# Kernel optimization log

Measured on AMD Instinct MI355X. Metric: run time of the kernel, lower is better.

## Reference

```python
import jax, jax.numpy as jnp
import numpy as np

B, S, D, H = 64, 512, 1024, 512
W_SEG, T_SEG, C_SEG = 96, 24, 128  # words, tables, columns per example (padded/fixed)


def setup_inputs() -> dict:
    key = jax.random.key(0)
    ks = jax.random.split(key, 8)
    return {
        "q_enc": jax.random.normal(ks[0], (B, S, D), dtype=jnp.float32),
        "W_sub": jax.random.normal(ks[1], (D, H), dtype=jnp.float32) * 0.02,
        "W_tab": jax.random.normal(ks[2], (D, H), dtype=jnp.float32) * 0.02,
        "W_col": jax.random.normal(ks[3], (D, H), dtype=jnp.float32) * 0.02,
        "no_entry": jax.random.normal(ks[4], (H,), dtype=jnp.float32) * 0.02,
        "word_seg": jax.random.randint(ks[5], (B, S), 0, W_SEG, dtype=jnp.int32),
        "table_seg": jax.random.randint(ks[6], (B, S), 0, T_SEG, dtype=jnp.int32),
        "col_seg": jax.random.randint(ks[7], (B, S), 0, C_SEG, dtype=jnp.int32),
    }


def _segsum(x, ids, n):
    # ragged range-sum over token axis: torch.sum(q_enc[b, st:ed, :], dim=0)
    return jax.vmap(lambda xb, ib: jax.ops.segment_sum(xb, ib, num_segments=n))(x, ids)


def reference(q_enc, W_sub, W_tab, W_col, no_entry, word_seg, table_seg, col_seg):
    word_vecs = _segsum(q_enc, word_seg, W_SEG)     # [B, W, D]
    tab_vecs = _segsum(q_enc, table_seg, T_SEG)     # [B, T, D]
    col_vecs = _segsum(q_enc, col_seg, C_SEG)       # [B, C, D]
    # SubtreeEncoder / SchemaEncoder abstracted as tanh-linear D -> H
    sub = jnp.tanh(word_vecs @ W_sub)               # [B, W, H] encoded subtrees
    tab = jnp.tanh(tab_vecs @ W_tab)                # [B, T, H]
    col = jnp.tanh(col_vecs @ W_col)                # [B, C, H]
    ne = jnp.broadcast_to(no_entry, (q_enc.shape[0], 1, no_entry.shape[0]))
    entity = jnp.concatenate([tab, col, ne], axis=1)  # [B, T+C+1, H]
    # per-example mm + softmax over entities
    att = jax.nn.softmax(jnp.einsum('bwh,beh->bwe', sub, entity), axis=-1)
    return att
```

## Files before the change

### kernel.cpp

```cpp
#include <hip/hip_runtime.h>
#include <hip/hip_bf16.h>
#include <math.h>

#define B_ 64
#define S_ 512
#define D_ 1024
#define H_ 512
#define WSEG 96
#define TSEG 24
#define CSEG 128
#define NSEG (WSEG + TSEG + CSEG)
#define ESEG (TSEG + CSEG + 1)
#define EPAD 160

typedef _Float16 f16x8 __attribute__((ext_vector_type(8)));
typedef _Float16 f16x4 __attribute__((ext_vector_type(4)));
typedef float f32x4 __attribute__((ext_vector_type(4)));

#define GL16(g, l)                                                      \
  __builtin_amdgcn_global_load_lds(                                     \
      (const __attribute__((address_space(1))) void*)(g),               \
      (__attribute__((address_space(3))) void*)(l), 16, 0, 0)

__device__ inline float tanh_fast(float x) {
  const float xc = fminf(12.f, fmaxf(-12.f, x));
  const float e = __expf(2.f * xc);
  return (e - 1.f) * __builtin_amdgcn_rcpf(e + 1.f);
}

__global__ __launch_bounds__(512) void setup_kernel(
    const int* __restrict__ wseg, const int* __restrict__ tseg,
    const int* __restrict__ cseg, const float* __restrict__ Ws,
    const float* __restrict__ Wt_, const float* __restrict__ Wc,
    const float* __restrict__ ne, int* __restrict__ lw, int* __restrict__ lt,
    int* __restrict__ lc, int* __restrict__ meta, _Float16* __restrict__ Wt16,
    _Float16* __restrict__ ent) {
  __shared__ int wid[S_], tid_[S_], cid[S_];
  __shared__ int cw[WSEG], ct[TSEG], ccnt[CSEG];
  __shared__ float tile[64][65];
  const int blk = blockIdx.x;
  const int t = threadIdx.x;

  if (blk < 64) {
    const int b = blk;
    const int myw = wseg[b * S_ + t];
    const int myt = tseg[b * S_ + t];
    const int myc = cseg[b * S_ + t];
    wid[t] = myw;
    tid_[t] = myt;
    cid[t] = myc;
    if (t < WSEG) cw[t] = 0;
    if (t < TSEG) ct[t] = 0;
    if (t < CSEG) ccnt[t] = 0;
    __syncthreads();

    atomicAdd(&cw[myw], 1);
    atomicAdd(&ct[myt], 1);
    atomicAdd(&ccnt[myc], 1);
    __syncthreads();

    if (t == 0) {
      int r = 0;
      for (int i = 0; i < WSEG; ++i) {
        const int c = cw[i];
        meta[b * NSEG + i] = r | (c << 16);
        cw[i] = r;
        r += c;
      }
      r = 0;
      for (int i = 0; i < TSEG; ++i) {
        const int c = ct[i];
        meta[b * NSEG + WSEG + i] = r | (c << 16);
        ct[i] = r;
        r += c;
      }
      r = 0;
      for (int i = 0; i < CSEG; ++i) {
        const int c = ccnt[i];
        meta[b * NSEG + WSEG + TSEG + i] = r | (c << 16);
        ccnt[i] = r;
        r += c;
      }
    }
    __syncthreads();

    int rw = 0, rt = 0, rc = 0;
    for (int s = 0; s < S_; ++s) {
      const int below = (s < t) ? 1 : 0;
      rw += below & (wid[s] == myw);
      rt += below & (tid_[s] == myt);
      rc += below & (cid[s] == myc);
    }
    lw[b * S_ + cw[myw] + rw] = t;
    lt[b * S_ + ct[myt] + rt] = t;
    lc[b * S_ + ccnt[myc] + rc] = t;
  } else if (blk < 448) {
    const int blk2 = blk - 64;
    const int z = blk2 >> 7;
    const int rem = blk2 & 127;
    const int k0 = (rem >> 3) * 64;
    const int n0 = (rem & 7) * 64;
    const float* W = (z == 0) ? Ws : ((z == 1) ? Wt_ : Wc);
    const int tx = t & 63, ty = (t >> 6) & 3;

    if (t < 256) {
#pragma unroll
      for (int i = 0; i < 16; ++i) {
        const int kl = i * 4 + ty;
        tile[kl][tx] = W[(size_t)(k0 + kl) * H_ + n0 + tx];
      }
    }
    __syncthreads();
    if (t < 256) {
      _Float16* oh = Wt16 + (size_t)z * H_ * D_;
#pragma unroll
      for (int i = 0; i < 16; ++i) {
        const int nl = i * 4 + ty;
        oh[(size_t)(n0 + nl) * D_ + k0 + tx] = (_Float16)tile[tx][nl];
      }
    }
  } else {
    const int b = blk - 448;
    ent[((size_t)b * EPAD + 152) * H_ + t] = (_Float16)ne[t];
#pragma unroll
    for (int r = 153; r < EPAD; ++r)
      ent[((size_t)b * EPAD + r) * H_ + t] = (_Float16)0.f;
  }
}

__global__ __launch_bounds__(256) void gather_rows_kernel(
    const float* __restrict__ q, const int* __restrict__ lw,
    const int* __restrict__ lt, const int* __restrict__ lc,
    const int* __restrict__ meta, _Float16* __restrict__ A) {
  const int t = threadIdx.x;
  const int bid = blockIdx.x;
  const int r = (bid & 7) * (B_ * NSEG / 8) + (bid >> 3);
  const int b = r / NSEG;
  const int seg = r % NSEG;

  const int m = meta[r];
  const int start = m & 0xFFFF;
  const int count = m >> 16;

  const int* list;
  int arow;
  if (seg < WSEG) {
    list = lw;
    arow = b * WSEG + seg;
  } else if (seg < WSEG + TSEG) {
    list = lt;
    arow = B_ * WSEG + b * TSEG + (seg - WSEG);
  } else {
    list = lc;
    arow = B_ * (WSEG + TSEG) + b * CSEG + (seg - WSEG - TSEG);
  }
  const int* lp = list + b * S_ + start;

  const float* qb = q + (size_t)b * S_ * D_;
  float4 acc = make_float4(0.f, 0.f, 0.f, 0.f);
  int i = 0;
  for (; i + 4 <= count; i += 4) {
    const int s0 = lp[i], s1 = lp[i + 1], s2 = lp[i + 2], s3 = lp[i + 3];
    const float4 a0 = *(const float4*)(qb + (size_t)s0 * D_ + (t << 2));
    const float4 a1 = *(const float4*)(qb + (size_t)s1 * D_ + (t << 2));
    const float4 a2 = *(const float4*)(qb + (size_t)s2 * D_ + (t << 2));
    const float4 a3 = *(const float4*)(qb + (size_t)s3 * D_ + (t << 2));
    acc.x += (a0.x + a1.x) + (a2.x + a3.x);
    acc.y += (a0.y + a1.y) + (a2.y + a3.y);
    acc.z += (a0.z + a1.z) + (a2.z + a3.z);
    acc.w += (a0.w + a1.w) + (a2.w + a3.w);
  }
  for (; i < count; ++i) {
    const float4 a = *(const float4*)(qb + (size_t)lp[i] * D_ + (t << 2));
    acc.x += a.x;
    acc.y += a.y;
    acc.z += a.z;
    acc.w += a.w;
  }
  const f16x4 hv = {(_Float16)acc.x, (_Float16)acc.y, (_Float16)acc.z,
                    (_Float16)acc.w};
  *(f16x4*)(A + (size_t)arow * D_ + (t << 2)) = hv;
}

__global__ __launch_bounds__(256) void gemm3_kernel(
    const _Float16* __restrict__ A, const _Float16* __restrict__ Wt16,
    _Float16* __restrict__ sub, _Float16* __restrict__ ent) {
  __shared__ __align__(16) char smem[32768];
  char* sA = smem;
  char* sB = smem + 16384;

  const int tid = threadIdx.x;
  const int wid = tid >> 6;
  const int lane = tid & 63;
  const int lin = blockIdx.x + blockIdx.y * 4;
  const int logical = (lin & 7) * 62 + (lin >> 3);
  const int m0 = (logical >> 2) * 128;
  const int n0 = (logical & 3) * 128;
  const int id = (m0 < B_ * WSEG) ? 0 : ((m0 < B_ * (WSEG + TSEG)) ? 1 : 2);

  const _Float16* B_g = Wt16 + (size_t)id * H_ * D_ + (size_t)n0 * D_;
  const _Float16* A_g = A + (size_t)m0 * D_;

  const int rsub = lane >> 3;
  const int csrc = (lane & 7) ^ rsub;

  const int wr = wid >> 1, wc = wid & 1;
  const int arow0 = wr * 64 + (lane & 15);
  const int brow0 = wc * 64 + (lane & 15);
  const int cbase = (lane >> 4) * 16;
  const int sw = (lane & 7) << 4;

  f32x4 acc[4][4] = {};

#pragma unroll 1
  for (int kt = 0; kt < D_ / 64; ++kt) {
    __syncthreads();
    const size_t kofs = (size_t)kt * 64 + (size_t)csrc * 8;
#pragma unroll
    for (int j = 0; j < 4; ++j) {
      const int i = wid * 4 + j;
      const size_t grow = (size_t)(i * 8 + rsub) * D_ + kofs;
      GL16(A_g + grow, sA + i * 1024);
      GL16(B_g + grow, sB + i * 1024);
    }
    __syncthreads();

#pragma unroll
    for (int ks = 0; ks < 2; ++ks) {
      const int cc = ((cbase + ks * 64) ^ sw);
      f16x8 a[4], bv[4];
#pragma unroll
      for (int mi = 0; mi < 4; ++mi)
        a[mi] = *(const f16x8*)(sA + (arow0 + mi * 16) * 128 + cc);
#pragma unroll
      for (int ni = 0; ni < 4; ++ni)
        bv[ni] = *(const f16x8*)(sB + (brow0 + ni * 16) * 128 + cc);
#pragma unroll
      for (int mi = 0; mi < 4; ++mi)
#pragma unroll
        for (int ni = 0; ni < 4; ++ni)
          acc[mi][ni] = __builtin_amdgcn_mfma_f32_16x16x32_f16(
              a[mi], bv[ni], acc[mi][ni], 0, 0, 0);
    }
  }

  const int rowb = m0 + wr * 64 + (lane >> 4) * 4;
  const int colb = n0 + wc * 64 + (lane & 15);
#pragma unroll
  for (int mi = 0; mi < 4; ++mi)
#pragma unroll
    for (int ni = 0; ni < 4; ++ni) {
      const f32x4 v = acc[mi][ni];
      const int col = colb + ni * 16;
#pragma unroll
      for (int r = 0; r < 4; ++r) {
        const int row = rowb + mi * 16 + r;
        const _Float16 val = (_Float16)tanh_fast(v[r]);
        if (id == 0) {
          sub[(size_t)row * H_ + col] = val;
        } else if (id == 1) {
          const int lr = row - B_ * WSEG;
          const int bb = lr / TSEG;
          const int rr = lr - bb * TSEG;
          ent[((size_t)bb * EPAD + rr) * H_ + col] = val;
        } else {
          const int lr = row - B_ * (WSEG + TSEG);
          const int bb = lr >> 7;
          const int rr = lr & 127;
          ent[((size_t)bb * EPAD + TSEG + rr) * H_ + col] = val;
        }
      }
    }
}

__global__ __launch_bounds__(192) void attn_mfma_kernel(
    const _Float16* __restrict__ sub, const _Float16* __restrict__ ent,
    float* __restrict__ out) {
  __shared__ __align__(16) char smem[30720];
  char* sS = smem;
  char* sE = smem + 6144;

  const int tid = threadIdx.x;
  const int wid = tid >> 6;
  const int lane = tid & 63;
  const int b = blockIdx.x >> 1;
  const int half = blockIdx.x & 1;

  const _Float16* S_g = sub + ((size_t)b * WSEG + half * 48) * H_;
  const _Float16* E_g = ent + (size_t)b * EPAD * H_;

  const int rsub = lane >> 3;
  const int csrc = (lane & 7) ^ rsub;

  const int arow0 = wid * 16 + (lane & 15);
  const int brow0 = lane & 15;
  const int cbase = (lane >> 4) * 16;
  const int sw = (lane & 7) << 4;

  f32x4 acc[10] = {};

#pragma unroll 1
  for (int kt = 0; kt < H_ / 64; ++kt) {
    __syncthreads();
    const size_t kofs = (size_t)kt * 64 + (size_t)csrc * 8;
#pragma unroll
    for (int j = 0; j < 9; ++j) {
      const int ig = wid * 9 + j;
      if (ig < 6) {
        GL16(S_g + (size_t)(ig * 8 + rsub) * H_ + kofs, sS + ig * 1024);
      } else if (ig < 26) {
        const int i = ig - 6;
        GL16(E_g + (size_t)(i * 8 + rsub) * H_ + kofs, sE + i * 1024);
      }
    }
    __syncthreads();

#pragma unroll
    for (int ks = 0; ks < 2; ++ks) {
      const int cc = ((cbase + ks * 64) ^ sw);
      const f16x8 a = *(const f16x8*)(sS + arow0 * 128 + cc);
#pragma unroll
      for (int ni = 0; ni < 10; ++ni) {
        const f16x8 bv = *(const f16x8*)(sE + (brow0 + ni * 16) * 128 + cc);
        acc[ni] = __builtin_amdgcn_mfma_f32_16x16x32_f16(a, bv, acc[ni], 0, 0,
                                                         0);
      }
    }
  }

  __syncthreads();
  float (*lg)[EPAD] = (float(*)[EPAD])smem;
  const int rowb = wid * 16 + (lane >> 4) * 4;
  const int colb = lane & 15;
#pragma unroll
  for (int ni = 0; ni < 10; ++ni) {
    const f32x4 v = acc[ni];
#pragma unroll
    for (int r = 0; r < 4; ++r) lg[rowb + r][colb + ni * 16] = v[r];
  }
  __syncthreads();

  for (int r = wid; r < 48; r += 3) {
    const float x0 = lg[r][lane];
    const float x1 = lg[r][lane + 64];
    const bool has2 = (lane + 128) < ESEG;
    const float x2 = has2 ? lg[r][lane + 128] : -INFINITY;
    float m = fmaxf(fmaxf(x0, x1), x2);
#pragma unroll
    for (int off = 32; off >= 1; off >>= 1) m = fmaxf(m, __shfl_xor(m, off, 64));
    const float p0 = expf(x0 - m);
    const float p1 = expf(x1 - m);
    const float p2 = has2 ? expf(x2 - m) : 0.f;
    float ssum = p0 + p1 + p2;
#pragma unroll
    for (int off = 32; off >= 1; off >>= 1) ssum += __shfl_xor(ssum, off, 64);
    const float inv = 1.f / ssum;
    float* ob = out + ((size_t)(b * WSEG + half * 48 + r)) * ESEG;
    ob[lane] = p0 * inv;
    ob[lane + 64] = p1 * inv;
    if (has2) ob[lane + 128] = p2 * inv;
  }
}

extern "C" void kernel_launch(void* const* d_in, const int* in_sizes, int n_in,
                              void* d_out, int out_size, void* d_ws,
                              size_t ws_size, hipStream_t stream) {
  const float* q = (const float*)d_in[0];
  const float* Wsub = (const float*)d_in[1];
  const float* Wtab = (const float*)d_in[2];
  const float* Wcol = (const float*)d_in[3];
  const float* ne = (const float*)d_in[4];
  const int* wseg = (const int*)d_in[5];
  const int* tseg = (const int*)d_in[6];
  const int* cseg = (const int*)d_in[7];
  float* out = (float*)d_out;

  char* w = (char*)d_ws;
  _Float16* A = (_Float16*)(w);
  _Float16* ent = (_Float16*)(w + 32505856);
  _Float16* Wt16 = (_Float16*)(w + 42991616);
  _Float16* sub = (_Float16*)(w + 46137344);
  int* lw = (int*)(w + 52428800);
  int* lt = (int*)(w + 52559872);
  int* lc = (int*)(w + 52690944);
  int* meta = (int*)(w + 52822016);

  setup_kernel<<<512, 512, 0, stream>>>(wseg, tseg, cseg, Wsub, Wtab, Wcol,
                                        ne, lw, lt, lc, meta, Wt16, ent);
  gather_rows_kernel<<<B_ * NSEG, 256, 0, stream>>>(q, lw, lt, lc, meta, A);
  gemm3_kernel<<<dim3(4, 124), 256, 0, stream>>>(A, Wt16, sub, ent);
  attn_mfma_kernel<<<B_ * 2, 192, 0, stream>>>(sub, ent, out);
}
```

Before: 110.2 us.

## Fuse setup and gather kernels, replace index lists with per-block ballot scans

Removes the setup kernel's counting, prefix-scan and list-building phase. Each gather block now scans the 512 segment ids of its example with wave ballots and sums the matching q rows directly. Weight transpose and entity padding run as extra blocks in the same launch, which drops one kernel launch and the dependency between the two front kernels. In exchange every gather block rereads all 512 ids and runs a serial bitmask loop with divergent conditional loads, where before it read a compact list.

```diff
diff --git a/kernel.cpp b/kernel.cpp
--- a/kernel.cpp
+++ b/kernel.cpp
@@ -28,154 +28,103 @@
   return (e - 1.f) * __builtin_amdgcn_rcpf(e + 1.f);
 }
 
-__global__ __launch_bounds__(512) void setup_kernel(
-    const int* __restrict__ wseg, const int* __restrict__ tseg,
-    const int* __restrict__ cseg, const float* __restrict__ Ws,
-    const float* __restrict__ Wt_, const float* __restrict__ Wc,
-    const float* __restrict__ ne, int* __restrict__ lw, int* __restrict__ lt,
-    int* __restrict__ lc, int* __restrict__ meta, _Float16* __restrict__ Wt16,
-    _Float16* __restrict__ ent) {
-  __shared__ int wid[S_], tid_[S_], cid[S_];
-  __shared__ int cw[WSEG], ct[TSEG], ccnt[CSEG];
+__global__ __launch_bounds__(256) void fused_front_kernel(
+    const float* __restrict__ q, const int* __restrict__ wseg,
+    const int* __restrict__ tseg, const int* __restrict__ cseg,
+    const float* __restrict__ Ws, const float* __restrict__ Wt_,
+    const float* __restrict__ Wc, const float* __restrict__ ne,
+    _Float16* __restrict__ Wt16, _Float16* __restrict__ ent,
+    _Float16* __restrict__ A) {
   __shared__ float tile[64][65];
   const int blk = blockIdx.x;
   const int t = threadIdx.x;
 
-  if (blk < 64) {
-    const int b = blk;
-    const int myw = wseg[b * S_ + t];
-    const int myt = tseg[b * S_ + t];
-    const int myc = cseg[b * S_ + t];
-    wid[t] = myw;
-    tid_[t] = myt;
-    cid[t] = myc;
-    if (t < WSEG) cw[t] = 0;
-    if (t < TSEG) ct[t] = 0;
-    if (t < CSEG) ccnt[t] = 0;
-    __syncthreads();
-
-    atomicAdd(&cw[myw], 1);
-    atomicAdd(&ct[myt], 1);
-    atomicAdd(&ccnt[myc], 1);
-    __syncthreads();
-
-    if (t == 0) {
-      int r = 0;
-      for (int i = 0; i < WSEG; ++i) {
-        const int c = cw[i];
-        meta[b * NSEG + i] = r | (c << 16);
-        cw[i] = r;
-        r += c;
-      }
-      r = 0;
-      for (int i = 0; i < TSEG; ++i) {
-        const int c = ct[i];
-        meta[b * NSEG + WSEG + i] = r | (c << 16);
-        ct[i] = r;
-        r += c;
-      }
-      r = 0;
-      for (int i = 0; i < CSEG; ++i) {
-        const int c = ccnt[i];
-        meta[b * NSEG + WSEG + TSEG + i] = r | (c << 16);
-        ccnt[i] = r;
-        r += c;
-      }
-    }
-    __syncthreads();
-
-    int rw = 0, rt = 0, rc = 0;
-    for (int s = 0; s < S_; ++s) {
-      const int below = (s < t) ? 1 : 0;
-      rw += below & (wid[s] == myw);
-      rt += below & (tid_[s] == myt);
-      rc += below & (cid[s] == myc);
-    }
-    lw[b * S_ + cw[myw] + rw] = t;
-    lt[b * S_ + ct[myt] + rt] = t;
-    lc[b * S_ + ccnt[myc] + rc] = t;
-  } else if (blk < 448) {
-    const int blk2 = blk - 64;
-    const int z = blk2 >> 7;
-    const int rem = blk2 & 127;
+  if (blk < 384) {
+    const int z = blk >> 7;
+    const int rem = blk & 127;
     const int k0 = (rem >> 3) * 64;
     const int n0 = (rem & 7) * 64;
     const float* W = (z == 0) ? Ws : ((z == 1) ? Wt_ : Wc);
-    const int tx = t & 63, ty = (t >> 6) & 3;
-
-    if (t < 256) {
-#pragma unroll
-      for (int i = 0; i < 16; ++i) {
-        const int kl = i * 4 + ty;
-        tile[kl][tx] = W[(size_t)(k0 + kl) * H_ + n0 + tx];
-      }
-    }
-    __syncthreads();
-    if (t < 256) {
-      _Float16* oh = Wt16 + (size_t)z * H_ * D_;
-#pragma unroll
-      for (int i = 0; i < 16; ++i) {
-        const int nl = i * 4 + ty;
-        oh[(size_t)(n0 + nl) * D_ + k0 + tx] = (_Float16)tile[tx][nl];
-      }
-    }
-  } else {
-    const int b = blk - 448;
-    ent[((size_t)b * EPAD + 152) * H_ + t] = (_Float16)ne[t];
-#pragma unroll
-    for (int r = 153; r < EPAD; ++r)
-      ent[((size_t)b * EPAD + r) * H_ + t] = (_Float16)0.f;
-  }
-}
-
-__global__ __launch_bounds__(256) void gather_rows_kernel(
-    const float* __restrict__ q, const int* __restrict__ lw,
-    const int* __restrict__ lt, const int* __restrict__ lc,
-    const int* __restrict__ meta, _Float16* __restrict__ A) {
-  const int t = threadIdx.x;
-  const int bid = blockIdx.x;
-  const int r = (bid & 7) * (B_ * NSEG / 8) + (bid >> 3);
+    const int tx = t & 63, ty = t >> 6;
+
+#pragma unroll
+    for (int i = 0; i < 16; ++i) {
+      const int kl = i * 4 + ty;
+      tile[kl][tx] = W[(size_t)(k0 + kl) * H_ + n0 + tx];
+    }
+    __syncthreads();
+    _Float16* oh = Wt16 + (size_t)z * H_ * D_;
+#pragma unroll
+    for (int i = 0; i < 16; ++i) {
+      const int nl = i * 4 + ty;
+      oh[(size_t)(n0 + nl) * D_ + k0 + tx] = (_Float16)tile[tx][nl];
+    }
+    return;
+  }
+  if (blk < 448) {
+    const int b = blk - 384;
+#pragma unroll
+    for (int hh = 0; hh < 2; ++hh) {
+      const int h = t + hh * 256;
+      ent[((size_t)b * EPAD + 152) * H_ + h] = (_Float16)ne[h];
+#pragma unroll
+      for (int r = 153; r < EPAD; ++r)
+        ent[((size_t)b * EPAD + r) * H_ + h] = (_Float16)0.f;
+    }
+    return;
+  }
+
+  const int g = blk - 448;
+  const int r = (g & 7) * (B_ * NSEG / 8) + (g >> 3);
   const int b = r / NSEG;
   const int seg = r % NSEG;
 
-  const int m = meta[r];
-  const int start = m & 0xFFFF;
-  const int count = m >> 16;
-
-  const int* list;
-  int arow;
+  const int* ids;
+  int target, arow;
   if (seg < WSEG) {
-    list = lw;
+    ids = wseg;
+    target = seg;
     arow = b * WSEG + seg;
   } else if (seg < WSEG + TSEG) {
-    list = lt;
+    ids = tseg;
+    target = seg - WSEG;
     arow = B_ * WSEG + b * TSEG + (seg - WSEG);
   } else {
-    list = lc;
+    ids = cseg;
+    target = seg - WSEG - TSEG;
     arow = B_ * (WSEG + TSEG) + b * CSEG + (seg - WSEG - TSEG);
   }
-  const int* lp = list + b * S_ + start;
+  ids += b * S_;
 
   const float* qb = q + (size_t)b * S_ * D_;
+  const int lane = t & 63;
   float4 acc = make_float4(0.f, 0.f, 0.f, 0.f);
-  int i = 0;
-  for (; i + 4 <= count; i += 4) {
-    const int s0 = lp[i], s1 = lp[i + 1], s2 = lp[i + 2], s3 = lp[i + 3];
-    const float4 a0 = *(const float4*)(qb + (size_t)s0 * D_ + (t << 2));
-    const float4 a1 = *(const float4*)(qb + (size_t)s1 * D_ + (t << 2));
-    const float4 a2 = *(const float4*)(qb + (size_t)s2 * D_ + (t << 2));
-    const float4 a3 = *(const float4*)(qb + (size_t)s3 * D_ + (t << 2));
-    acc.x += (a0.x + a1.x) + (a2.x + a3.x);
-    acc.y += (a0.y + a1.y) + (a2.y + a3.y);
-    acc.z += (a0.z + a1.z) + (a2.z + a3.z);
-    acc.w += (a0.w + a1.w) + (a2.w + a3.w);
-  }
-  for (; i < count; ++i) {
-    const float4 a = *(const float4*)(qb + (size_t)lp[i] * D_ + (t << 2));
-    acc.x += a.x;
-    acc.y += a.y;
-    acc.z += a.z;
-    acc.w += a.w;
+
+#pragma unroll 1
+  for (int i = 0; i < 8; ++i) {
+    const int idv = ids[i * 64 + lane];
+    unsigned long long mask = __ballot(idv == target);
+    while (mask) {
+      int b0, b1 = -1, b2 = -1, b3 = -1;
+      b0 = __ffsll((long long)mask) - 1;
+      mask &= mask - 1;
+      if (mask) { b1 = __ffsll((long long)mask) - 1; mask &= mask - 1; }
+      if (mask) { b2 = __ffsll((long long)mask) - 1; mask &= mask - 1; }
+      if (mask) { b3 = __ffsll((long long)mask) - 1; mask &= mask - 1; }
+      const float4 a0 =
+          *(const float4*)(qb + (size_t)(i * 64 + b0) * D_ + (t << 2));
+      float4 a1, a2, a3;
+      if (b1 >= 0)
+        a1 = *(const float4*)(qb + (size_t)(i * 64 + b1) * D_ + (t << 2));
+      if (b2 >= 0)
+        a2 = *(const float4*)(qb + (size_t)(i * 64 + b2) * D_ + (t << 2));
+      if (b3 >= 0)
+        a3 = *(const float4*)(qb + (size_t)(i * 64 + b3) * D_ + (t << 2));
+      acc.x += a0.x; acc.y += a0.y; acc.z += a0.z; acc.w += a0.w;
+      if (b1 >= 0) { acc.x += a1.x; acc.y += a1.y; acc.z += a1.z; acc.w += a1.w; }
+      if (b2 >= 0) { acc.x += a2.x; acc.y += a2.y; acc.z += a2.z; acc.w += a2.w; }
+      if (b3 >= 0) { acc.x += a3.x; acc.y += a3.y; acc.z += a3.z; acc.w += a3.w; }
+    }
   }
   const f16x4 hv = {(_Float16)acc.x, (_Float16)acc.y, (_Float16)acc.z,
                     (_Float16)acc.w};
@@ -380,14 +329,9 @@
   _Float16* ent = (_Float16*)(w + 32505856);
   _Float16* Wt16 = (_Float16*)(w + 42991616);
   _Float16* sub = (_Float16*)(w + 46137344);
-  int* lw = (int*)(w + 52428800);
-  int* lt = (int*)(w + 52559872);
-  int* lc = (int*)(w + 52690944);
-  int* meta = (int*)(w + 52822016);
-
-  setup_kernel<<<512, 512, 0, stream>>>(wseg, tseg, cseg, Wsub, Wtab, Wcol,
-                                        ne, lw, lt, lc, meta, Wt16, ent);
-  gather_rows_kernel<<<B_ * NSEG, 256, 0, stream>>>(q, lw, lt, lc, meta, A);
+
+  fused_front_kernel<<<448 + B_ * NSEG, 256, 0, stream>>>(
+      q, wseg, tseg, cseg, Wsub, Wtab, Wcol, ne, Wt16, ent, A);
   gemm3_kernel<<<dim3(4, 124), 256, 0, stream>>>(A, Wt16, sub, ent);
   attn_mfma_kernel<<<B_ * 2, 192, 0, stream>>>(sub, ent, out);
 }
```

Measured after the change: 92.75 us. 15.9% less time.
